# Kernel optimization log

Hardware: AMD Instinct MI355X
Metric: run time of the kernel (lower is better)

Reference implementation:

```python
import jax, jax.numpy as jnp
import numpy as np

H, NH, L, S, B, V = 512, 8, 6, 2048, 2, 32000
DH = H // NH
EPS = 1e-5


def posenc(h, s):
    pos = jnp.arange(s, dtype=jnp.float32)[:, None]
    div = jnp.power(10000.0, jnp.arange(0, h, 2, dtype=jnp.float32) / h)
    pe = jnp.zeros((s, h), dtype=jnp.float32)
    pe = pe.at[:, 0::2].set(jnp.sin(pos / div))
    pe = pe.at[:, 1::2].set(jnp.cos(pos / div))
    return pe


def layernorm(x, g, b):
    mu = jnp.mean(x, axis=-1, keepdims=True)
    var = jnp.mean(jnp.square(x - mu), axis=-1, keepdims=True)
    return (x - mu) * jax.lax.rsqrt(var + EPS) * g + b


def setup_inputs() -> dict:
    key = jax.random.key(0)
    ks = jax.random.split(key, 16)
    sc = 0.02
    return {
        "src": jax.random.randint(ks[0], (B, S), 0, V),
        "mask": jnp.ones((B, 1, 1, S), dtype=jnp.int32),
        "emb": jax.random.normal(ks[1], (V, H), jnp.float32) * sc,
        "Wq": jax.random.normal(ks[2], (L, H, H), jnp.float32) * sc,
        "bq": jnp.zeros((L, H), jnp.float32),
        "Wk": jax.random.normal(ks[3], (L, H, H), jnp.float32) * sc,
        "bk": jnp.zeros((L, H), jnp.float32),
        "Wv": jax.random.normal(ks[4], (L, H, H), jnp.float32) * sc,
        "bv": jnp.zeros((L, H), jnp.float32),
        "Wo": jax.random.normal(ks[5], (L, H, H), jnp.float32) * sc,
        "bo": jnp.zeros((L, H), jnp.float32),
        "gamma": jnp.ones((L, H), jnp.float32),
        "beta": jnp.zeros((L, H), jnp.float32),
        "W1": jax.random.normal(ks[6], (L, H, 4 * H), jnp.float32) * sc,
        "b1": jnp.zeros((L, 4 * H), jnp.float32),
        "W2": jax.random.normal(ks[7], (L, 4 * H, H), jnp.float32) * sc,
        "b2": jnp.zeros((L, H), jnp.float32),
    }


def reference(src, mask, emb, Wq, bq, Wk, bk, Wv, bv, Wo, bo, gamma, beta, W1, b1, W2, b2):
    x = emb[src] + posenc(H, S)[None, :, :]  # [B,S,H]
    for i in range(L):
        q = (x @ Wq[i] + bq[i]).reshape(B, S, NH, DH).transpose(0, 2, 1, 3)
        k = (x @ Wk[i] + bk[i]).reshape(B, S, NH, DH).transpose(0, 2, 1, 3)
        v = (x @ Wv[i] + bv[i]).reshape(B, S, NH, DH).transpose(0, 2, 1, 3)
        scores = jnp.einsum("bhqd,bhkd->bhqk", q, k) / jnp.sqrt(jnp.float32(DH))
        scores = jnp.where(mask == 0, jnp.float32(-1e20), scores)
        attn = jax.nn.softmax(scores, axis=-1)
        av = jnp.einsum("bhqk,bhkd->bhqd", attn, v)
        attn_out = av.transpose(0, 2, 1, 3).reshape(B, S, H) @ Wo[i] + bo[i]
        # NOTE: same LayerNorm params applied to both sublayers (as in source)
        res = x + layernorm(attn_out, gamma[i], beta[i])
        ffn = jax.nn.relu(res @ W1[i] + b1[i]) @ W2[i] + b2[i]
        x = res + layernorm(ffn, gamma[i], beta[i])
    return x
```

## Files before the change

kernel.cpp:

```cpp
#include <hip/hip_runtime.h>
#include <math.h>

#define HDIM 512
#define NHEAD 8
#define NLAYER 6
#define SEQ 2048
#define BATCH 2
#define DHEAD 64
#define TOKENS (BATCH*SEQ)
#define FFND (4*HDIM)
#define QSTR 1536

typedef unsigned short u16;
typedef __attribute__((ext_vector_type(8))) short short8;
typedef __attribute__((ext_vector_type(4))) float f32x4;

__device__ __forceinline__ u16 f2b(float f) {
  unsigned u = __float_as_uint(f);
  u += 0x7FFFu + ((u >> 16) & 1u);
  return (u16)(u >> 16);
}

__device__ __forceinline__ void gload_lds16(const u16* g, u16* l) {
  __builtin_amdgcn_global_load_lds((const __attribute__((address_space(1))) void*)g,
                                   (__attribute__((address_space(3))) void*)l, 16, 0, 0);
}

__global__ void embed_pe(const int* __restrict__ src, const float* __restrict__ emb,
                         float* __restrict__ X, u16* __restrict__ Xb) {
  int tok = blockIdx.x;
  int lane = threadIdx.x;
  int s = tok & (SEQ - 1);
  int c0 = lane * 8;
  const float* e = emb + (long)src[tok] * HDIM + c0;
  float v[8];
#pragma unroll
  for (int j = 0; j < 8; j++) {
    int c = c0 + j;
    float arg = (float)s * exp2f(-(float)(c & ~1) * 0.02595256917f);
    v[j] = e[j] + ((c & 1) ? cosf(arg) : sinf(arg));
  }
  float* xp = X + (long)tok * HDIM + c0;
#pragma unroll
  for (int j = 0; j < 8; j++) xp[j] = v[j];
  u16 hb[8];
#pragma unroll
  for (int j = 0; j < 8; j++) hb[j] = f2b(v[j]);
  uint4 pk;
  pk.x = hb[0] | ((unsigned)hb[1] << 16);
  pk.y = hb[2] | ((unsigned)hb[3] << 16);
  pk.z = hb[4] | ((unsigned)hb[5] << 16);
  pk.w = hb[6] | ((unsigned)hb[7] << 16);
  *(uint4*)(Xb + (long)tok * HDIM + c0) = pk;
}

__global__ __launch_bounds__(256) void prep_weights(
    const float* __restrict__ Wq, const float* __restrict__ Wk, const float* __restrict__ Wv,
    const float* __restrict__ Wo, const float* __restrict__ W1, const float* __restrict__ W2,
    const float* __restrict__ bq, const float* __restrict__ bk, const float* __restrict__ bv,
    u16* __restrict__ Wqkvt, u16* __restrict__ Wot, u16* __restrict__ W1t, u16* __restrict__ W2t,
    float* __restrict__ bqkv) {
  int t = blockIdx.x;
  int tid = threadIdx.x;
  if (t == 768) {
    for (int i = tid; i < 1536; i += 256)
      bqkv[i] = (i < 512) ? bq[i] : (i < 1024) ? bk[i - 512] : bv[i - 1024];
    return;
  }
  const float* src; u16* dst; int K, N, kt, nt; long drow0 = 0;
  if (t < 192)      { int m = t / 64, r = t % 64; src = (m==0)?Wq:(m==1)?Wk:Wv; dst = Wqkvt; drow0 = (long)m*512; K=512;  N=512;  kt=r/8;  nt=r%8; }
  else if (t < 256) { int r = t - 192; src = Wo; dst = Wot; K=512;  N=512;  kt=r/8;  nt=r%8; }
  else if (t < 512) { int r = t - 256; src = W1; dst = W1t; K=512;  N=2048; kt=r/32; nt=r%32; }
  else              { int r = t - 512; src = W2; dst = W2t; K=2048; N=512;  kt=r/8;  nt=r%8; }
  __shared__ __align__(16) u16 Lt[64 * 72];
  int kl = tid >> 2;
#pragma unroll
  for (int rr = 0; rr < 4; rr++) {
    int cl = (tid & 3) * 4 + rr * 16;
    float4 v = *(const float4*)(src + (long)(kt * 64 + kl) * N + nt * 64 + cl);
    Lt[(cl + 0) * 72 + kl] = f2b(v.x);
    Lt[(cl + 1) * 72 + kl] = f2b(v.y);
    Lt[(cl + 2) * 72 + kl] = f2b(v.z);
    Lt[(cl + 3) * 72 + kl] = f2b(v.w);
  }
  __syncthreads();
  int nl = tid >> 2;
  int kc = (tid & 3) * 16;
  u16* dp = dst + (drow0 + nt * 64 + nl) * (long)K + kt * 64 + kc;
  *(uint4*)dp       = *(const uint4*)&Lt[nl * 72 + kc];
  *(uint4*)(dp + 8) = *(const uint4*)&Lt[nl * 72 + kc + 8];
}

__global__ __launch_bounds__(256) void vtranspose(const u16* __restrict__ QKV,
                                                  u16* __restrict__ Vtb) {
  __shared__ __align__(16) u16 Lt[64 * 72];
  int tid = threadIdx.x;
  int bh = blockIdx.y, b = bh >> 3, h = bh & 7;
  int s0 = blockIdx.x * 64;
  const u16* vsrc = QKV + (long)(b * SEQ + s0) * QSTR + 1024 + h * DHEAD;
  int key = tid >> 2, dc = (tid & 3) * 16;
  const u16* vp = vsrc + (long)key * QSTR + dc;
  uint4 v0 = *(const uint4*)vp;
  uint4 v1 = *(const uint4*)(vp + 8);
  unsigned vr[8] = { v0.x, v0.y, v0.z, v0.w, v1.x, v1.y, v1.z, v1.w };
#pragma unroll
  for (int j = 0; j < 8; j++) {
    Lt[(dc + 2 * j) * 72 + key]     = (u16)vr[j];
    Lt[(dc + 2 * j + 1) * 72 + key] = (u16)(vr[j] >> 16);
  }
  __syncthreads();
  int d = tid >> 2, kc = (tid & 3) * 16;
  u16* dst = Vtb + ((long)bh * DHEAD + d) * SEQ + s0 + kc;
  *(uint4*)dst       = *(const uint4*)&Lt[d * 72 + kc];
  *(uint4*)(dst + 8) = *(const uint4*)&Lt[d * 72 + kc + 8];
}

template <int BN, int KSPLIT, bool RELU, bool WF32, bool WB16>
__global__ __launch_bounds__(256) void gemm_tn(const u16* __restrict__ A,
                                               const u16* __restrict__ Bt,
                                               const float* __restrict__ bias,
                                               float* __restrict__ Cf,
                                               u16* __restrict__ Cb,
                                               int M, int N, int K) {
  constexpr int NF = BN / 32;
  __shared__ __align__(16) u16 As[2][128 * 32];
  __shared__ __align__(16) u16 Bs[2][BN * 32];
  int tid = threadIdx.x;
  int wave = tid >> 6, lane = tid & 63;
  int ln = lane & 15, hi = lane >> 4;
  int wm = wave >> 1, wn = wave & 1;
  int m0 = blockIdx.y * 128, n0 = blockIdx.x * BN;
  int z = (KSPLIT > 1) ? blockIdx.z : 0;
  int Ks = K / KSPLIT;
  const u16* Ab = A + z * Ks;
  const u16* Bb = Bt + z * Ks;

  f32x4 acc[4][NF] = {};

  int srow = lane >> 2;
  int skc  = (lane & 3) * 8;

  auto issue = [&](int kt, int buf) {
    int k0 = kt * 32;
#pragma unroll
    for (int j = 0; j < 2; j++) {
      int row = (wave * 2 + j) * 16 + srow;
      gload_lds16(Ab + (long)(m0 + row) * K + k0 + skc, &As[buf][row * 32 + skc]);
    }
#pragma unroll
    for (int j = 0; j < BN / 64; j++) {
      int row = (wave * (BN / 64) + j) * 16 + srow;
      gload_lds16(Bb + (long)(n0 + row) * K + k0 + skc, &Bs[buf][row * 32 + skc]);
    }
  };

  int NT = Ks / 32;
  issue(0, 0);
  __syncthreads();
  for (int kt = 0; kt < NT; kt++) {
    int buf = kt & 1;
    if (kt + 1 < NT) issue(kt + 1, buf ^ 1);
    short8 af[4], bf[NF];
#pragma unroll
    for (int mt = 0; mt < 4; mt++)
      af[mt] = *(const short8*)&As[buf][(wm * 64 + mt * 16 + ln) * 32 + 8 * hi];
#pragma unroll
    for (int nt = 0; nt < NF; nt++)
      bf[nt] = *(const short8*)&Bs[buf][(wn * (BN / 2) + nt * 16 + ln) * 32 + 8 * hi];
#pragma unroll
    for (int mt = 0; mt < 4; mt++)
#pragma unroll
      for (int nt = 0; nt < NF; nt++)
        acc[mt][nt] = __builtin_amdgcn_mfma_f32_16x16x32_bf16(af[mt], bf[nt], acc[mt][nt], 0, 0, 0);
    __syncthreads();
  }

  float* Cz = WF32 ? (Cf + (long)z * M * N) : nullptr;
#pragma unroll
  for (int mt = 0; mt < 4; mt++)
#pragma unroll
    for (int nt = 0; nt < NF; nt++)
#pragma unroll
      for (int r = 0; r < 4; r++) {
        int row = m0 + wm * 64 + mt * 16 + hi * 4 + r;
        int col = n0 + wn * (BN / 2) + nt * 16 + ln;
        float v = acc[mt][nt][r];
        if (KSPLIT == 1 || z == 0) v += bias[col];
        if (RELU) v = fmaxf(v, 0.0f);
        if (WF32) Cz[(long)row * N + col] = v;
        if (WB16) Cb[(long)row * N + col] = f2b(v);
      }
}

__global__ __launch_bounds__(256) void attention(const u16* __restrict__ QKV,
                                                 const u16* __restrict__ Vtb,
                                                 const int* __restrict__ mask,
                                                 u16* __restrict__ Og) {
  __shared__ __align__(16) u16 Ks[2][2][64 * 32];
  __shared__ __align__(16) u16 Vs[2][2][64 * 32];
  __shared__ __align__(16) u16 P[4 * 16 * 72];
  int tid = threadIdx.x, w = tid >> 6, lane = tid & 63;
  int ln = lane & 15, hi = lane >> 4;
  int bh = blockIdx.y, b = bh >> 3, h = bh & 7;
  int q0 = blockIdx.x * 64 + w * 16;
  const u16* qbase = QKV + (long)b * SEQ * QSTR + h * DHEAD;
  const u16* kbase = qbase + 512;
  const u16* vtbase = Vtb + (long)bh * DHEAD * SEQ;
  const int* mrow = mask + b * SEQ;
  u16* Pw = P + w * 16 * 72;

  short8 qf[2];
#pragma unroll
  for (int ks = 0; ks < 2; ks++)
    qf[ks] = *(const short8*)(qbase + (long)(q0 + ln) * QSTR + ks * 32 + 8 * hi);

  f32x4 o[4] = {};
  float lst[4] = {0.0f, 0.0f, 0.0f, 0.0f};

  int srow = w * 16 + (lane >> 2);
  int sc = (lane & 3) * 8;

  auto issue = [&](int t, int buf) {
    long kk = (long)t * 64;
    const u16* kg = kbase + (kk + srow) * QSTR + sc;
    gload_lds16(kg,      &Ks[buf][0][srow * 32 + sc]);
    gload_lds16(kg + 32, &Ks[buf][1][srow * 32 + sc]);
    const u16* vg = vtbase + (long)srow * SEQ + kk + sc;
    gload_lds16(vg,      &Vs[buf][0][srow * 32 + sc]);
    gload_lds16(vg + 32, &Vs[buf][1][srow * 32 + sc]);
  };

  const int NT = SEQ / 64;
  issue(0, 0);
  __syncthreads();
  for (int t = 0; t < NT; t++) {
    int buf = t & 1;
    if (t + 1 < NT) issue(t + 1, buf ^ 1);
    int k0 = t * 64;

    f32x4 s[4] = {};
#pragma unroll
    for (int ks = 0; ks < 2; ks++)
#pragma unroll
      for (int nt = 0; nt < 4; nt++) {
        short8 bf = *(const short8*)&Ks[buf][ks][(nt * 16 + ln) * 32 + 8 * hi];
        s[nt] = __builtin_amdgcn_mfma_f32_16x16x32_bf16(qf[ks], bf, s[nt], 0, 0, 0);
      }
    int mv[4];
#pragma unroll
    for (int nt = 0; nt < 4; nt++) mv[nt] = mrow[k0 + nt * 16 + ln];
#pragma unroll
    for (int r = 0; r < 4; r++) {
#pragma unroll
      for (int nt = 0; nt < 4; nt++) {
        float p = (mv[nt] == 0) ? 0.0f : __expf(s[nt][r] * 0.125f);
        lst[r] += p;
        Pw[(hi * 4 + r) * 72 + ((nt * 16 + ln) ^ (8 * hi))] = f2b(p);
      }
    }
    short8 pa[2];
#pragma unroll
    for (int ka = 0; ka < 2; ka++)
      pa[ka] = *(const short8*)&Pw[ln * 72 + (ka * 32 + ((8 * hi) ^ (8 * (ln >> 2))))];
#pragma unroll
    for (int nt = 0; nt < 4; nt++) {
      short8 bv0 = *(const short8*)&Vs[buf][0][(nt * 16 + ln) * 32 + 8 * hi];
      short8 bv1 = *(const short8*)&Vs[buf][1][(nt * 16 + ln) * 32 + 8 * hi];
      o[nt] = __builtin_amdgcn_mfma_f32_16x16x32_bf16(pa[0], bv0, o[nt], 0, 0, 0);
      o[nt] = __builtin_amdgcn_mfma_f32_16x16x32_bf16(pa[1], bv1, o[nt], 0, 0, 0);
    }
    __syncthreads();
  }

#pragma unroll
  for (int r = 0; r < 4; r++) {
    float l = lst[r];
    l += __shfl_xor(l, 1);
    l += __shfl_xor(l, 2);
    l += __shfl_xor(l, 4);
    l += __shfl_xor(l, 8);
    lst[r] = 1.0f / l;
  }

  u16* obase = Og + (long)b * SEQ * HDIM + h * DHEAD;
#pragma unroll
  for (int r = 0; r < 4; r++) {
    int srow2 = q0 + hi * 4 + r;
#pragma unroll
    for (int nt = 0; nt < 4; nt++)
      obase[(long)srow2 * HDIM + nt * 16 + ln] = f2b(o[nt][r] * lst[r]);
  }
}

__global__ __launch_bounds__(256) void ln_residual(const float* __restrict__ Xin,
                                                   const float* __restrict__ T0,
                                                   const float* __restrict__ T1,
                                                   const float* __restrict__ gamma,
                                                   const float* __restrict__ beta,
                                                   float* __restrict__ Xout,
                                                   u16* __restrict__ Xb) {
  int tid = threadIdx.x, w = tid >> 6, lane = tid & 63;
  int row = blockIdx.x * 4 + w;
  const float* t0 = T0 + (long)row * HDIM;
  const float* t1 = T1 + (long)row * HDIM;
  int c0 = lane * 8;
  float v[8];
  {
    float4 a0 = *(const float4*)(t0 + c0);
    float4 b0 = *(const float4*)(t0 + c0 + 4);
    float4 a1 = *(const float4*)(t1 + c0);
    float4 b1 = *(const float4*)(t1 + c0 + 4);
    v[0] = a0.x + a1.x; v[1] = a0.y + a1.y; v[2] = a0.z + a1.z; v[3] = a0.w + a1.w;
    v[4] = b0.x + b1.x; v[5] = b0.y + b1.y; v[6] = b0.z + b1.z; v[7] = b0.w + b1.w;
  }
  float sum = 0.0f;
#pragma unroll
  for (int j = 0; j < 8; j++) sum += v[j];
#pragma unroll
  for (int off = 32; off; off >>= 1) sum += __shfl_xor(sum, off);
  float mu = sum * (1.0f / HDIM);
  float sq = 0.0f;
#pragma unroll
  for (int j = 0; j < 8; j++) { float d = v[j] - mu; sq += d * d; }
#pragma unroll
  for (int off = 32; off; off >>= 1) sq += __shfl_xor(sq, off);
  float rs = rsqrtf(sq * (1.0f / HDIM) + 1e-5f);
  const float* xin = Xin + (long)row * HDIM + c0;
  float* xout = Xout + (long)row * HDIM + c0;
  u16 hb[8];
#pragma unroll
  for (int j = 0; j < 8; j++) {
    int c = c0 + j;
    float y = xin[j] + (v[j] - mu) * rs * gamma[c] + beta[c];
    xout[j] = y;
    hb[j] = f2b(y);
  }
  uint4 pk;
  pk.x = hb[0] | ((unsigned)hb[1] << 16);
  pk.y = hb[2] | ((unsigned)hb[3] << 16);
  pk.z = hb[4] | ((unsigned)hb[5] << 16);
  pk.w = hb[6] | ((unsigned)hb[7] << 16);
  *(uint4*)(Xb + (long)row * HDIM + c0) = pk;
}

extern "C" void kernel_launch(void* const* d_in, const int* in_sizes, int n_in,
                              void* d_out, int out_size, void* d_ws, size_t ws_size,
                              hipStream_t stream) {
  const int*   src   = (const int*)d_in[0];
  const int*   mask  = (const int*)d_in[1];
  const float* emb   = (const float*)d_in[2];
  const float* Wq    = (const float*)d_in[3];
  const float* bq    = (const float*)d_in[4];
  const float* Wk    = (const float*)d_in[5];
  const float* bk    = (const float*)d_in[6];
  const float* Wv    = (const float*)d_in[7];
  const float* bv    = (const float*)d_in[8];
  const float* Wo    = (const float*)d_in[9];
  const float* bo    = (const float*)d_in[10];
  const float* gamma = (const float*)d_in[11];
  const float* beta  = (const float*)d_in[12];
  const float* W1    = (const float*)d_in[13];
  const float* b1    = (const float*)d_in[14];
  const float* W2    = (const float*)d_in[15];
  const float* b2    = (const float*)d_in[16];

  char* ws = (char*)d_ws;
  float* X     = (float*)(ws);
  u16*   Xb    = (u16*)(ws + (8ll << 20));
  u16*   QKVb  = (u16*)(ws + (12ll << 20));
  u16*   Mb    = (u16*)(ws + (12ll << 20));
  u16*   AVb   = (u16*)(ws + (24ll << 20));
  float* T     = (float*)(ws + (28ll << 20));
  u16*   Wqkvt = (u16*)(ws + (44ll << 20));
  u16*   Wot   = (u16*)(ws + (45ll << 20) + (512ll << 10));
  u16*   W1t   = (u16*)(ws + (46ll << 20));
  u16*   W2t   = (u16*)(ws + (48ll << 20));
  float* bqkv  = (float*)(ws + (50ll << 20));
  u16*   Vtb   = (u16*)(ws + (51ll << 20));
  float* T1    = T + (long)TOKENS * HDIM;

  embed_pe<<<dim3(TOKENS), dim3(64), 0, stream>>>(src, emb, X, Xb);

  for (int i = 0; i < NLAYER; i++) {
    long wo = (long)i * HDIM * HDIM;
    prep_weights<<<dim3(769), 256, 0, stream>>>(
        Wq + wo, Wk + wo, Wv + wo, Wo + wo,
        W1 + (long)i * HDIM * FFND, W2 + (long)i * FFND * HDIM,
        bq + i * HDIM, bk + i * HDIM, bv + i * HDIM,
        Wqkvt, Wot, W1t, W2t, bqkv);

    gemm_tn<128, 1, false, false, true><<<dim3(QSTR / 128, TOKENS / 128), 256, 0, stream>>>(
        Xb, Wqkvt, bqkv, nullptr, QKVb, TOKENS, QSTR, HDIM);

    vtranspose<<<dim3(SEQ / 64, BATCH * NHEAD), 256, 0, stream>>>(QKVb, Vtb);

    attention<<<dim3(SEQ / 64, BATCH * NHEAD), 256, 0, stream>>>(QKVb, Vtb, mask, AVb);

    gemm_tn<64, 2, false, true, false><<<dim3(HDIM / 64, TOKENS / 128, 2), 256, 0, stream>>>(
        AVb, Wot, bo + i * HDIM, T, nullptr, TOKENS, HDIM, HDIM);

    ln_residual<<<dim3(TOKENS / 4), 256, 0, stream>>>(X, T, T1, gamma + i * HDIM,
                                                      beta + i * HDIM, X, Xb);

    gemm_tn<128, 1, true, false, true><<<dim3(FFND / 128, TOKENS / 128), 256, 0, stream>>>(
        Xb, W1t, b1 + (long)i * FFND, nullptr, Mb, TOKENS, FFND, HDIM);

    gemm_tn<64, 2, false, true, false><<<dim3(HDIM / 64, TOKENS / 128, 2), 256, 0, stream>>>(
        Mb, W2t, b2 + i * HDIM, T, nullptr, TOKENS, HDIM, FFND);

    ln_residual<<<dim3(TOKENS / 4), 256, 0, stream>>>(X, T, T1, gamma + i * HDIM,
                                                      beta + i * HDIM, X, Xb);
  }

  hipMemcpyAsync(d_out, X, (size_t)TOKENS * HDIM * sizeof(float),
                 hipMemcpyDeviceToDevice, stream);
}
```

Baseline: 1.060 ms.

## Split attention over key halves with a combine kernel and transposed score layout

Attention now splits the key sequence into two halves across a third grid dimension, writing unnormalized fp32 partial outputs and row sums. A new combine kernel adds the halves, normalizes, and converts to bf16. Scores are computed transposed so each lane holds four consecutive keys, which lets the P tile be written with packed stores and without the old XOR swizzle. The integer mask is converted once to float and multiplied in. The point is to double the attention grid for better occupancy and cut per-element LDS stores, at the cost of an extra kernel launch and fp32 partial traffic. Without a running max, the split relies on unshifted exponentials, as the code before already did.

```diff
diff --git a/kernel.cpp b/kernel.cpp
--- a/kernel.cpp
+++ b/kernel.cpp
@@ -52,6 +52,11 @@
   pk.z = hb[4] | ((unsigned)hb[5] << 16);
   pk.w = hb[6] | ((unsigned)hb[7] << 16);
   *(uint4*)(Xb + (long)tok * HDIM + c0) = pk;
+}
+
+__global__ void mask2f(const int* __restrict__ mask, float* __restrict__ maskf) {
+  int i = blockIdx.x * 256 + threadIdx.x;
+  maskf[i] = (mask[i] == 0) ? 0.0f : 1.0f;
 }
 
 __global__ __launch_bounds__(256) void prep_weights(
@@ -194,20 +199,22 @@
 
 __global__ __launch_bounds__(256) void attention(const u16* __restrict__ QKV,
                                                  const u16* __restrict__ Vtb,
-                                                 const int* __restrict__ mask,
-                                                 u16* __restrict__ Og) {
+                                                 const float* __restrict__ maskf,
+                                                 float* __restrict__ Opart,
+                                                 float* __restrict__ Lpart) {
   __shared__ __align__(16) u16 Ks[2][2][64 * 32];
   __shared__ __align__(16) u16 Vs[2][2][64 * 32];
-  __shared__ __align__(16) u16 P[4 * 16 * 72];
+  __shared__ __align__(16) u16 P[4 * 16 * 80];
   int tid = threadIdx.x, w = tid >> 6, lane = tid & 63;
   int ln = lane & 15, hi = lane >> 4;
   int bh = blockIdx.y, b = bh >> 3, h = bh & 7;
+  int z = blockIdx.z;
   int q0 = blockIdx.x * 64 + w * 16;
   const u16* qbase = QKV + (long)b * SEQ * QSTR + h * DHEAD;
   const u16* kbase = qbase + 512;
   const u16* vtbase = Vtb + (long)bh * DHEAD * SEQ;
-  const int* mrow = mask + b * SEQ;
-  u16* Pw = P + w * 16 * 72;
+  const float* mbase = maskf + b * SEQ + z * (SEQ / 2);
+  u16* Pw = P + w * 16 * 80;
 
   short8 qf[2];
 #pragma unroll
@@ -215,13 +222,13 @@
     qf[ks] = *(const short8*)(qbase + (long)(q0 + ln) * QSTR + ks * 32 + 8 * hi);
 
   f32x4 o[4] = {};
-  float lst[4] = {0.0f, 0.0f, 0.0f, 0.0f};
+  float lsum = 0.0f;
 
   int srow = w * 16 + (lane >> 2);
   int sc = (lane & 3) * 8;
 
   auto issue = [&](int t, int buf) {
-    long kk = (long)t * 64;
+    long kk = (long)z * (SEQ / 2) + t * 64;
     const u16* kg = kbase + (kk + srow) * QSTR + sc;
     gload_lds16(kg,      &Ks[buf][0][srow * 32 + sc]);
     gload_lds16(kg + 32, &Ks[buf][1][srow * 32 + sc]);
@@ -230,7 +237,7 @@
     gload_lds16(vg + 32, &Vs[buf][1][srow * 32 + sc]);
   };
 
-  const int NT = SEQ / 64;
+  const int NT = (SEQ / 2) / 64;
   issue(0, 0);
   __syncthreads();
   for (int t = 0; t < NT; t++) {
@@ -243,25 +250,29 @@
     for (int ks = 0; ks < 2; ks++)
 #pragma unroll
       for (int nt = 0; nt < 4; nt++) {
-        short8 bf = *(const short8*)&Ks[buf][ks][(nt * 16 + ln) * 32 + 8 * hi];
-        s[nt] = __builtin_amdgcn_mfma_f32_16x16x32_bf16(qf[ks], bf, s[nt], 0, 0, 0);
+        short8 kf = *(const short8*)&Ks[buf][ks][(nt * 16 + ln) * 32 + 8 * hi];
+        s[nt] = __builtin_amdgcn_mfma_f32_16x16x32_bf16(kf, qf[ks], s[nt], 0, 0, 0);
       }
-    int mv[4];
-#pragma unroll
-    for (int nt = 0; nt < 4; nt++) mv[nt] = mrow[k0 + nt * 16 + ln];
-#pragma unroll
-    for (int r = 0; r < 4; r++) {
-#pragma unroll
-      for (int nt = 0; nt < 4; nt++) {
-        float p = (mv[nt] == 0) ? 0.0f : __expf(s[nt][r] * 0.125f);
-        lst[r] += p;
-        Pw[(hi * 4 + r) * 72 + ((nt * 16 + ln) ^ (8 * hi))] = f2b(p);
+#pragma unroll
+    for (int nt = 0; nt < 4; nt++) {
+      float4 mf = *(const float4*)(mbase + k0 + nt * 16 + hi * 4);
+      float mfa[4] = { mf.x, mf.y, mf.z, mf.w };
+      u16 hb[4];
+#pragma unroll
+      for (int r = 0; r < 4; r++) {
+        float p = __expf(s[nt][r] * 0.125f) * mfa[r];
+        lsum += p;
+        hb[r] = f2b(p);
       }
+      uint2 pk;
+      pk.x = hb[0] | ((unsigned)hb[1] << 16);
+      pk.y = hb[2] | ((unsigned)hb[3] << 16);
+      *(uint2*)&Pw[ln * 80 + nt * 16 + hi * 4] = pk;
     }
     short8 pa[2];
 #pragma unroll
     for (int ka = 0; ka < 2; ka++)
-      pa[ka] = *(const short8*)&Pw[ln * 72 + (ka * 32 + ((8 * hi) ^ (8 * (ln >> 2))))];
+      pa[ka] = *(const short8*)&Pw[ln * 80 + ka * 32 + 8 * hi];
 #pragma unroll
     for (int nt = 0; nt < 4; nt++) {
       short8 bv0 = *(const short8*)&Vs[buf][0][(nt * 16 + ln) * 32 + 8 * hi];
@@ -272,24 +283,46 @@
     __syncthreads();
   }
 
-#pragma unroll
-  for (int r = 0; r < 4; r++) {
-    float l = lst[r];
-    l += __shfl_xor(l, 1);
-    l += __shfl_xor(l, 2);
-    l += __shfl_xor(l, 4);
-    l += __shfl_xor(l, 8);
-    lst[r] = 1.0f / l;
-  }
-
-  u16* obase = Og + (long)b * SEQ * HDIM + h * DHEAD;
+  lsum += __shfl_xor(lsum, 16);
+  lsum += __shfl_xor(lsum, 32);
+  if (lane < 16)
+    Lpart[(long)z * BATCH * NHEAD * SEQ + (long)bh * SEQ + q0 + ln] = lsum;
+
+  float* obase = Opart + (long)z * TOKENS * HDIM + (long)b * SEQ * HDIM + h * DHEAD;
 #pragma unroll
   for (int r = 0; r < 4; r++) {
     int srow2 = q0 + hi * 4 + r;
 #pragma unroll
     for (int nt = 0; nt < 4; nt++)
-      obase[(long)srow2 * HDIM + nt * 16 + ln] = f2b(o[nt][r] * lst[r]);
-  }
+      obase[(long)srow2 * HDIM + nt * 16 + ln] = o[nt][r];
+  }
+}
+
+__global__ __launch_bounds__(256) void attn_combine(const float* __restrict__ Opart,
+                                                    const float* __restrict__ Lpart,
+                                                    u16* __restrict__ AVb) {
+  int tid = threadIdx.x, w = tid >> 6, lane = tid & 63;
+  int row = blockIdx.x * 4 + w;
+  int b = row >> 11, s = row & (SEQ - 1);
+  int c0 = lane * 8, h = c0 >> 6;
+  const float* o0 = Opart + (long)row * HDIM + c0;
+  const float* o1 = Opart + (long)TOKENS * HDIM + (long)row * HDIM + c0;
+  float l0 = Lpart[(long)(b * NHEAD + h) * SEQ + s];
+  float l1 = Lpart[(long)BATCH * NHEAD * SEQ + (long)(b * NHEAD + h) * SEQ + s];
+  float inv = 1.0f / (l0 + l1);
+  float4 a0 = *(const float4*)o0, b0 = *(const float4*)(o0 + 4);
+  float4 a1 = *(const float4*)o1, b1 = *(const float4*)(o1 + 4);
+  u16 hb[8];
+  hb[0] = f2b((a0.x + a1.x) * inv); hb[1] = f2b((a0.y + a1.y) * inv);
+  hb[2] = f2b((a0.z + a1.z) * inv); hb[3] = f2b((a0.w + a1.w) * inv);
+  hb[4] = f2b((b0.x + b1.x) * inv); hb[5] = f2b((b0.y + b1.y) * inv);
+  hb[6] = f2b((b0.z + b1.z) * inv); hb[7] = f2b((b0.w + b1.w) * inv);
+  uint4 pk;
+  pk.x = hb[0] | ((unsigned)hb[1] << 16);
+  pk.y = hb[2] | ((unsigned)hb[3] << 16);
+  pk.z = hb[4] | ((unsigned)hb[5] << 16);
+  pk.w = hb[6] | ((unsigned)hb[7] << 16);
+  *(uint4*)(AVb + (long)row * HDIM + c0) = pk;
 }
 
 __global__ __launch_bounds__(256) void ln_residual(const float* __restrict__ Xin,
@@ -377,9 +410,12 @@
   u16*   W2t   = (u16*)(ws + (48ll << 20));
   float* bqkv  = (float*)(ws + (50ll << 20));
   u16*   Vtb   = (u16*)(ws + (51ll << 20));
+  float* Lpart = (float*)(ws + (55ll << 20));
+  float* maskf = (float*)(ws + (55ll << 20) + (512ll << 10));
   float* T1    = T + (long)TOKENS * HDIM;
 
   embed_pe<<<dim3(TOKENS), dim3(64), 0, stream>>>(src, emb, X, Xb);
+  mask2f<<<dim3(BATCH * SEQ / 256), 256, 0, stream>>>(mask, maskf);
 
   for (int i = 0; i < NLAYER; i++) {
     long wo = (long)i * HDIM * HDIM;
@@ -394,7 +430,9 @@
 
     vtranspose<<<dim3(SEQ / 64, BATCH * NHEAD), 256, 0, stream>>>(QKVb, Vtb);
 
-    attention<<<dim3(SEQ / 64, BATCH * NHEAD), 256, 0, stream>>>(QKVb, Vtb, mask, AVb);
+    attention<<<dim3(SEQ / 64, BATCH * NHEAD, 2), 256, 0, stream>>>(QKVb, Vtb, maskf, T, Lpart);
+
+    attn_combine<<<dim3(TOKENS / 4), 256, 0, stream>>>(T, Lpart, AVb);
 
     gemm_tn<64, 2, false, true, false><<<dim3(HDIM / 64, TOKENS / 128, 2), 256, 0, stream>>>(
         AVb, Wot, bo + i * HDIM, T, nullptr, TOKENS, HDIM, HDIM);
```

Result: slower. 1.089 ms (+2.7%).

## Transpose QK MFMA operands to vectorize P stores and precompute float mask

Applied to the files above, without the earlier changes.

The attention kernel now computes S^T by swapping the MFMA operands. Each lane then holds four consecutive keys for one query, which lets it pack P into 8-byte LDS stores with padded stride 88 instead of the XOR swizzle, and reduces the row sum to one scalar per lane. The int mask becomes a float multiplier, precomputed once by a new kernel and loaded as float4. The grid is also reordered so that blocks with the same query tile but different heads run adjacently. The aim is to cut the scalar LDS stores, compare/select work and shuffle-reduction overhead in the softmax path, at the cost of an extra small kernel and workspace buffer.

```diff
diff --git a/kernel.cpp b/kernel.cpp
--- a/kernel.cpp
+++ b/kernel.cpp
@@ -10,6 +10,7 @@
 #define TOKENS (BATCH*SEQ)
 #define FFND (4*HDIM)
 #define QSTR 1536
+#define PSTR 88
 
 typedef unsigned short u16;
 typedef __attribute__((ext_vector_type(8))) short short8;
@@ -52,6 +53,11 @@
   pk.z = hb[4] | ((unsigned)hb[5] << 16);
   pk.w = hb[6] | ((unsigned)hb[7] << 16);
   *(uint4*)(Xb + (long)tok * HDIM + c0) = pk;
+}
+
+__global__ void mask2f(const int* __restrict__ mask, float* __restrict__ maskf) {
+  int i = blockIdx.x * 256 + threadIdx.x;
+  maskf[i] = (mask[i] == 0) ? 0.0f : 1.0f;
 }
 
 __global__ __launch_bounds__(256) void prep_weights(
@@ -194,20 +200,20 @@
 
 __global__ __launch_bounds__(256) void attention(const u16* __restrict__ QKV,
                                                  const u16* __restrict__ Vtb,
-                                                 const int* __restrict__ mask,
+                                                 const float* __restrict__ maskf,
                                                  u16* __restrict__ Og) {
   __shared__ __align__(16) u16 Ks[2][2][64 * 32];
   __shared__ __align__(16) u16 Vs[2][2][64 * 32];
-  __shared__ __align__(16) u16 P[4 * 16 * 72];
+  __shared__ __align__(16) u16 P[4 * 16 * PSTR];
   int tid = threadIdx.x, w = tid >> 6, lane = tid & 63;
   int ln = lane & 15, hi = lane >> 4;
-  int bh = blockIdx.y, b = bh >> 3, h = bh & 7;
-  int q0 = blockIdx.x * 64 + w * 16;
+  int bh = blockIdx.x, b = bh >> 3, h = bh & 7;
+  int q0 = blockIdx.y * 64 + w * 16;
   const u16* qbase = QKV + (long)b * SEQ * QSTR + h * DHEAD;
   const u16* kbase = qbase + 512;
   const u16* vtbase = Vtb + (long)bh * DHEAD * SEQ;
-  const int* mrow = mask + b * SEQ;
-  u16* Pw = P + w * 16 * 72;
+  const float* mbase = maskf + b * SEQ;
+  u16* Pw = P + w * 16 * PSTR;
 
   short8 qf[2];
 #pragma unroll
@@ -215,7 +221,7 @@
     qf[ks] = *(const short8*)(qbase + (long)(q0 + ln) * QSTR + ks * 32 + 8 * hi);
 
   f32x4 o[4] = {};
-  float lst[4] = {0.0f, 0.0f, 0.0f, 0.0f};
+  float lsum = 0.0f;
 
   int srow = w * 16 + (lane >> 2);
   int sc = (lane & 3) * 8;
@@ -243,25 +249,29 @@
     for (int ks = 0; ks < 2; ks++)
 #pragma unroll
       for (int nt = 0; nt < 4; nt++) {
-        short8 bf = *(const short8*)&Ks[buf][ks][(nt * 16 + ln) * 32 + 8 * hi];
-        s[nt] = __builtin_amdgcn_mfma_f32_16x16x32_bf16(qf[ks], bf, s[nt], 0, 0, 0);
+        short8 kf = *(const short8*)&Ks[buf][ks][(nt * 16 + ln) * 32 + 8 * hi];
+        s[nt] = __builtin_amdgcn_mfma_f32_16x16x32_bf16(kf, qf[ks], s[nt], 0, 0, 0);
       }
-    int mv[4];
-#pragma unroll
-    for (int nt = 0; nt < 4; nt++) mv[nt] = mrow[k0 + nt * 16 + ln];
-#pragma unroll
-    for (int r = 0; r < 4; r++) {
-#pragma unroll
-      for (int nt = 0; nt < 4; nt++) {
-        float p = (mv[nt] == 0) ? 0.0f : __expf(s[nt][r] * 0.125f);
-        lst[r] += p;
-        Pw[(hi * 4 + r) * 72 + ((nt * 16 + ln) ^ (8 * hi))] = f2b(p);
+#pragma unroll
+    for (int nt = 0; nt < 4; nt++) {
+      float4 mf = *(const float4*)(mbase + k0 + nt * 16 + hi * 4);
+      float mfa[4] = { mf.x, mf.y, mf.z, mf.w };
+      u16 hb[4];
+#pragma unroll
+      for (int r = 0; r < 4; r++) {
+        float p = __expf(s[nt][r] * 0.125f) * mfa[r];
+        lsum += p;
+        hb[r] = f2b(p);
       }
+      uint2 pk;
+      pk.x = hb[0] | ((unsigned)hb[1] << 16);
+      pk.y = hb[2] | ((unsigned)hb[3] << 16);
+      *(uint2*)&Pw[ln * PSTR + nt * 16 + hi * 4] = pk;
     }
     short8 pa[2];
 #pragma unroll
     for (int ka = 0; ka < 2; ka++)
-      pa[ka] = *(const short8*)&Pw[ln * 72 + (ka * 32 + ((8 * hi) ^ (8 * (ln >> 2))))];
+      pa[ka] = *(const short8*)&Pw[ln * PSTR + ka * 32 + 8 * hi];
 #pragma unroll
     for (int nt = 0; nt < 4; nt++) {
       short8 bv0 = *(const short8*)&Vs[buf][0][(nt * 16 + ln) * 32 + 8 * hi];
@@ -272,15 +282,12 @@
     __syncthreads();
   }
 
-#pragma unroll
-  for (int r = 0; r < 4; r++) {
-    float l = lst[r];
-    l += __shfl_xor(l, 1);
-    l += __shfl_xor(l, 2);
-    l += __shfl_xor(l, 4);
-    l += __shfl_xor(l, 8);
-    lst[r] = 1.0f / l;
-  }
+  lsum += __shfl_xor(lsum, 16);
+  lsum += __shfl_xor(lsum, 32);
+  float inv[4];
+#pragma unroll
+  for (int r = 0; r < 4; r++)
+    inv[r] = 1.0f / __shfl(lsum, hi * 4 + r);
 
   u16* obase = Og + (long)b * SEQ * HDIM + h * DHEAD;
 #pragma unroll
@@ -288,7 +295,7 @@
     int srow2 = q0 + hi * 4 + r;
 #pragma unroll
     for (int nt = 0; nt < 4; nt++)
-      obase[(long)srow2 * HDIM + nt * 16 + ln] = f2b(o[nt][r] * lst[r]);
+      obase[(long)srow2 * HDIM + nt * 16 + ln] = f2b(o[nt][r] * inv[r]);
   }
 }
 
@@ -377,9 +384,11 @@
   u16*   W2t   = (u16*)(ws + (48ll << 20));
   float* bqkv  = (float*)(ws + (50ll << 20));
   u16*   Vtb   = (u16*)(ws + (51ll << 20));
+  float* maskf = (float*)(ws + (55ll << 20));
   float* T1    = T + (long)TOKENS * HDIM;
 
   embed_pe<<<dim3(TOKENS), dim3(64), 0, stream>>>(src, emb, X, Xb);
+  mask2f<<<dim3(BATCH * SEQ / 256), 256, 0, stream>>>(mask, maskf);
 
   for (int i = 0; i < NLAYER; i++) {
     long wo = (long)i * HDIM * HDIM;
@@ -394,7 +403,7 @@
 
     vtranspose<<<dim3(SEQ / 64, BATCH * NHEAD), 256, 0, stream>>>(QKVb, Vtb);
 
-    attention<<<dim3(SEQ / 64, BATCH * NHEAD), 256, 0, stream>>>(QKVb, Vtb, mask, AVb);
+    attention<<<dim3(BATCH * NHEAD, SEQ / 64), 256, 0, stream>>>(QKVb, Vtb, maskf, AVb);
 
     gemm_tn<64, 2, false, true, false><<<dim3(HDIM / 64, TOKENS / 128, 2), 256, 0, stream>>>(
         AVb, Wot, bo + i * HDIM, T, nullptr, TOKENS, HDIM, HDIM);
```

After: 1.070 ms. About the same (+1.0%).
